# Kernel tuning notes

Hardware: AMD Instinct MI355X
Metric: run time of the kernel (lower is better)

## Reference

```python
import jax, jax.numpy as jnp
import numpy as np

# ---- config (from init_kwargs) ----
PRE_NMS_THRESH = 0.05
PRE_NMS_TOP_N = 1000
NMS_THRESH = 0.6
FPN_POST_NMS_TOP_N = 100
MIN_SIZE = 0.0
FPN_STRIDES = (8.0, 16.0, 32.0, 64.0, 128.0)
TO_REMOVE = 1.0

M = 2097152   # total FPN points over the batch
N = 16        # images
C = 11        # classes incl. background column (zeroed)


def setup_inputs() -> dict:
    key = jax.random.key(0)
    k1, k2, k3, k4, k5, k6 = jax.random.split(key, 6)
    locations = jax.random.uniform(k1, (M, 2), jnp.float32) * 1024.0
    box_cls = jax.random.normal(k2, (M, C), jnp.float32) * 2.0
    box_regression = jax.random.uniform(k3, (M, 4), jnp.float32) * 4.0
    centerness = jax.random.normal(k4, (M, 1), jnp.float32)
    levels = jax.random.randint(k5, (M,), 0, len(FPN_STRIDES), jnp.int32)
    batch_indices = jnp.sort(jax.random.randint(k6, (M,), 0, N, jnp.int32))
    image_sizes = jnp.tile(jnp.array([[800, 1333]], jnp.int32), (N, 1))  # (h, w)
    return dict(locations=locations, levels=levels, batch_indices=batch_indices,
                box_cls=box_cls, box_regression=box_regression,
                centerness=centerness, image_sizes=image_sizes)


def _iou_matrix(b):
    x1, y1, x2, y2 = b[:, 0], b[:, 1], b[:, 2], b[:, 3]
    area = jnp.clip(x2 - x1 + TO_REMOVE, 0.0) * jnp.clip(y2 - y1 + TO_REMOVE, 0.0)
    xx1 = jnp.maximum(x1[:, None], x1[None, :])
    yy1 = jnp.maximum(y1[:, None], y1[None, :])
    xx2 = jnp.minimum(x2[:, None], x2[None, :])
    yy2 = jnp.minimum(y2[:, None], y2[None, :])
    inter = jnp.clip(xx2 - xx1 + TO_REMOVE, 0.0) * jnp.clip(yy2 - yy1 + TO_REMOVE, 0.0)
    return inter / jnp.maximum(area[:, None] + area[None, :] - inter, 1e-9)


def _greedy_nms(iou, keep0):
    # boxes assumed sorted by descending score; keep0 = validity mask
    K = keep0.shape[0]
    idx = jnp.arange(K)
    def step(keep, i):
        sup = (iou[i] > NMS_THRESH) & (idx > i) & keep[i]
        return keep & ~sup, None
    keep, _ = jax.lax.scan(step, keep0, jnp.arange(K))
    return keep


def _fcos_post(locations, box_cls, box_regression, centerness,
               levels, batch_indices, image_sizes):
    strides = jnp.asarray(FPN_STRIDES, box_regression.dtype)
    reg = box_regression * strides[levels][:, None]          # norm_reg_targets=True
    scores = jax.nn.sigmoid(box_cls) * jax.nn.sigmoid(centerness)  # [M,C]
    scores = scores.at[:, -1].set(0.0)                       # kill background column
    boxes_all = jnp.concatenate([locations - reg[:, :2],
                                 locations + reg[:, 2:]], axis=-1)  # [M,4]

    def per_image(args):
        i, hw = args
        m = (batch_indices == i)[:, None] & (scores > PRE_NMS_THRESH)
        flat = jnp.where(m, scores, 0.0).reshape(-1)          # [M*C]
        topv, topi = jax.lax.top_k(flat, PRE_NMS_TOP_N)       # sorted desc
        pt = topi // C
        cl = (topi % C + 1).astype(jnp.int32)                 # labels = class + 1
        b = boxes_all[pt]                                     # [K,4]
        v0 = topv > 0.0                                       # pad entries -> invalid
        sc = jnp.sqrt(jnp.where(v0, topv, 1.0)) * v0          # sqrt(score), safe at pads
        h = hw[0].astype(b.dtype); w = hw[1].astype(b.dtype)
        x1 = jnp.clip(b[:, 0], 0.0, w - TO_REMOVE)            # clip_to_image
        y1 = jnp.clip(b[:, 1], 0.0, h - TO_REMOVE)
        x2 = jnp.clip(b[:, 2], 0.0, w - TO_REMOVE)
        y2 = jnp.clip(b[:, 3], 0.0, h - TO_REMOVE)
        b = jnp.stack([x1, y1, x2, y2], axis=-1)
        ws = x2 - x1 + TO_REMOVE; hs = y2 - y1 + TO_REMOVE    # remove_small_boxes
        keep0 = v0 & (ws >= MIN_SIZE) & (hs >= MIN_SIZE)
        # class-aware NMS via coordinate offset trick
        max_coord = jnp.max(jnp.where(keep0[:, None], b, 0.0))
        boff = jax.lax.stop_gradient(b + (cl.astype(b.dtype) * (max_coord + 1.0))[:, None])
        keep = _greedy_nms(_iou_matrix(boff), keep0)
        sck = jnp.where(keep, sc, 0.0)
        fv, fi = jax.lax.top_k(sck, FPN_POST_NMS_TOP_N)       # fpn_post_nms_top_n
        return b[fi], fv, cl[fi], fv > 0.0

    boxes_o, scores_o, labels_o, valid_o = jax.lax.map(
        per_image, (jnp.arange(N), image_sizes))
    return boxes_o, scores_o, labels_o, valid_o


def reference(locations, levels, batch_indices, box_cls, box_regression,
              centerness, image_sizes):
    return _fcos_post(locations, box_cls, box_regression, centerness,
                      levels, batch_indices, image_sizes)
```

## Files before the change

kernel.cpp:

```cpp
#include <hip/hip_runtime.h>
#include <math.h>

#pragma clang fp contract(off)

#define MPTS   2097152
#define NIMG   16
#define NCLS   11
#define CUTB   0x3F000000u
#define PREB   0x3F4CCC00u
#define BSAFE  620
#define PRECAP 14336
#define NB2    1026
#define NB2P   1040
#define MARG   96u
#define CAP    4096
#define TOPN   1000
#define OUTN   100
#define LCAP   64

typedef unsigned long long u64;

#define SUPW_PER_IMG 8704
__device__ __forceinline__ int chunk_base(int c) {
    return 64 * (16 * c - (c * (c - 1)) / 2);
}

__device__ inline float sigx(float x) {
    float e = (float)exp(-(double)x);
    return 1.0f / (1.0f + e);
}
__device__ inline float sigf(float x) {
    float e = __expf(-x);
    return __builtin_amdgcn_rcpf(1.0f + e);
}
__device__ inline float bfr(float x) {
    unsigned u = __float_as_uint(x);
    unsigned r = (u + 0x7FFFu + ((u >> 16) & 1u)) & 0xFFFF0000u;
    return __uint_as_float(r);
}
__device__ __forceinline__ u64 rdlane64(u64 v, int l) {
    unsigned lo = (unsigned)__builtin_amdgcn_readlane((int)(unsigned)(v & 0xFFFFFFFFull), l);
    unsigned hi = (unsigned)__builtin_amdgcn_readlane((int)(unsigned)(v >> 32), l);
    return ((u64)hi << 32) | (u64)lo;
}

__global__ __launch_bounds__(1024)
void k_hist(const float4* __restrict__ cls4, const float* __restrict__ ctr,
            const int* __restrict__ batch, unsigned* __restrict__ ghist,
            unsigned* __restrict__ gcnt, unsigned* __restrict__ prerec) {
    __shared__ unsigned hist[NB2];
    __shared__ unsigned pA[512], pB[256];
    __shared__ unsigned cA, cB, bA;
    __shared__ int simg;
    const int F4  = MPTS * NCLS / 4;
    const int FPB = F4 / 512;
    int f0 = blockIdx.x * FPB;
    int t = threadIdx.x;
    for (int i = t; i < NB2; i += 1024) hist[i] = 0;
    if (t == 0) { simg = batch[(unsigned)(4u * (unsigned)f0) / NCLS]; cA = 0; cB = 0; }
    __syncthreads();
    int bi = simg;
    unsigned pc = 0xFFFFFFFFu;
    float sfc = 0.0f;
    int bc = 0;
    for (int f = f0 + t; f < f0 + FPB; f += 1024) {
        float4 v = cls4[f];
        float va[4] = {v.x, v.y, v.z, v.w};
        unsigned e0 = 4u * (unsigned)f;
        #pragma unroll
        for (int j = 0; j < 4; j++) {
            float ck = va[j];
            if (ck <= 0.0f) continue;
            unsigned e = e0 + (unsigned)j;
            unsigned p = e / NCLS;
            unsigned k = e - p * NCLS;
            if (k == 10u) continue;
            if (p != pc) {
                pc = p; sfc = sigf(ctr[p]); bc = batch[p];
            }
            unsigned fb = __float_as_uint(sigf(ck) * sfc);
            if (fb < CUTB) continue;
            unsigned bin = (fb - CUTB) >> 13;
            if (bin >= NB2) bin = NB2 - 1;
            if (bc == bi) atomicAdd(&hist[bin], 1u);
            else          atomicAdd(&ghist[(size_t)bc * NB2P + bin], 1u);
            if (fb >= PREB) {
                if (bc == bi) {
                    unsigned sl = atomicAdd(&cA, 1u);
                    if (sl < 512u) pA[sl] = e;
                    else {
                        unsigned pos = atomicAdd(&gcnt[bi * 16 + 8], 1u);
                        if (pos < PRECAP) prerec[(size_t)bi * PRECAP + pos] = e;
                    }
                } else {
                    unsigned sl = atomicAdd(&cB, 1u);
                    if (sl < 256u) pB[sl] = e;
                    else {
                        unsigned pos = atomicAdd(&gcnt[bc * 16 + 8], 1u);
                        if (pos < PRECAP) prerec[(size_t)bc * PRECAP + pos] = e;
                    }
                }
            }
        }
    }
    __syncthreads();
    unsigned* gh = ghist + (size_t)bi * NB2P;
    for (int i = t; i < NB2; i += 1024) {
        unsigned v2 = hist[i];
        if (v2) atomicAdd(&gh[i], v2);
    }
    if (t == 0) {
        unsigned nn = cA; if (nn > 512u) nn = 512u;
        cA = nn;
        bA = nn ? atomicAdd(&gcnt[bi * 16 + 8], nn) : 0u;
    }
    __syncthreads();
    for (unsigned i = t; i < cA; i += 1024) {
        unsigned pos = bA + i;
        if (pos < PRECAP) prerec[(size_t)bi * PRECAP + pos] = pA[i];
    }
    unsigned nb = cB; if (nb > 256u) nb = 256u;
    for (unsigned i = t; i < nb; i += 1024) {
        unsigned e2 = pB[i];
        int img2 = batch[e2 / NCLS];
        unsigned pos = atomicAdd(&gcnt[img2 * 16 + 8], 1u);
        if (pos < PRECAP) prerec[(size_t)img2 * PRECAP + pos] = e2;
    }
}

__global__ void k_thresh(const unsigned* __restrict__ ghist, unsigned* __restrict__ thrbuf,
                         unsigned* __restrict__ gcnt) {
    int img = blockIdx.x;
    const unsigned* h = ghist + (size_t)img * NB2P;
    __shared__ unsigned psum[256];
    int t = threadIdx.x;
    unsigned s = 0;
    int base = t * 5;
    for (int i = 0; i < 5; i++) { int b = base + i; if (b < NB2) s += h[b]; }
    psum[t] = s;
    __syncthreads();
    if (t == 0) {
        unsigned run = 0; int B = 0;
        for (int u = 205; u >= 0; u--) {
            if (run + psum[u] >= (unsigned)TOPN) {
                int btop = u * 5 + 4; if (btop > NB2 - 1) btop = NB2 - 1;
                for (int b = btop; b >= u * 5; b--) {
                    run += h[b];
                    if (run >= (unsigned)TOPN) { B = b; break; }
                }
                break;
            }
            run += psum[u];
        }
        unsigned TB = CUTB + ((unsigned)B << 13) - MARG;
        thrbuf[2 * img] = TB;
        thrbuf[2 * img + 1] = __float_as_uint(__uint_as_float(TB) * 0.998f);
        if (B < BSAFE || gcnt[img * 16 + 8] > PRECAP) atomicOr(&gcnt[1], 1u);
    }
}

__global__ __launch_bounds__(256)
void k_collect(const float4* __restrict__ cls4, const float* __restrict__ clsf,
               const float* __restrict__ ctr, const int* __restrict__ batch,
               const unsigned* __restrict__ thrbuf, unsigned* __restrict__ gcnt,
               const unsigned* __restrict__ prerec, unsigned long long* __restrict__ cand) {
    int t = threadIdx.x;
    if (gcnt[1] == 0u) {
        if (blockIdx.x >= 256) return;
        int img = blockIdx.x >> 4;
        int sub = blockIdx.x & 15;
        unsigned TB = thrbuf[2 * img];
        float scr = __uint_as_float(thrbuf[2 * img + 1]);
        unsigned n = gcnt[img * 16 + 8];
        __shared__ u64 l2[512];
        __shared__ unsigned c2, b2;
        if (t == 0) c2 = 0;
        __syncthreads();
        const unsigned* pr = prerec + (size_t)img * PRECAP;
        for (unsigned i = (unsigned)(sub * 256 + t); i < n; i += 4096) {
            unsigned e = pr[i];
            unsigned p = e / NCLS;
            float ck = clsf[e];
            float cgs = ctr[p];
            float sf = sigf(ck) * sigf(cgs);
            if (sf > scr) {
                float s = sigx(ck) * sigx(cgs);
                unsigned bits = __float_as_uint(s);
                if (bits >= TB && s > 0.05f) {
                    u64 key = ((u64)bits << 32) | (u64)(0xFFFFFFFFu - e);
                    unsigned sl = atomicAdd(&c2, 1u);
                    if (sl < 512u) l2[sl] = key;
                    else {
                        unsigned pos = atomicAdd(&gcnt[img * 16], 1u);
                        if (pos < CAP) cand[(size_t)img * CAP + pos] = key;
                    }
                }
            }
        }
        __syncthreads();
        if (t == 0) {
            unsigned nn = c2; if (nn > 512u) nn = 512u;
            c2 = nn;
            b2 = nn ? atomicAdd(&gcnt[img * 16], nn) : 0u;
        }
        __syncthreads();
        for (unsigned sl = t; sl < c2; sl += 256) {
            unsigned pos = b2 + sl;
            if (pos < CAP) cand[(size_t)img * CAP + pos] = l2[sl];
        }
        return;
    }
    __shared__ unsigned sTB[NIMG];
    __shared__ float sSCR[NIMG];
    __shared__ u64 lbuf[NIMG][LCAP];
    __shared__ unsigned lcnt[NIMG];
    __shared__ unsigned lbase[NIMG];
    if (t < NIMG) {
        sTB[t]  = thrbuf[2 * t];
        sSCR[t] = __uint_as_float(thrbuf[2 * t + 1]);
        lcnt[t] = 0;
    }
    __syncthreads();
    const int F4  = MPTS * NCLS / 4;
    const int FPB = F4 / 2048;
    int f0 = blockIdx.x * FPB;
    unsigned pc = 0xFFFFFFFFu;
    float cgs = 0.0f, sfc = 0.0f, sxc = 0.0f, scrc = 0.0f;
    bool havex = false;
    int bc = 0; unsigned TBc = 0;
    for (int f = f0 + t; f < f0 + FPB; f += 256) {
        float4 v = cls4[f];
        float va[4] = {v.x, v.y, v.z, v.w};
        unsigned e0 = 4u * (unsigned)f;
        #pragma unroll
        for (int j = 0; j < 4; j++) {
            float ck = va[j];
            if (ck <= -0.001f) continue;
            unsigned e = e0 + (unsigned)j;
            unsigned p = e / NCLS;
            unsigned k = e - p * NCLS;
            if (k == 10u) continue;
            if (p != pc) {
                pc = p; cgs = ctr[p]; bc = batch[p];
                sfc = sigf(cgs); havex = false;
                TBc = sTB[bc]; scrc = sSCR[bc];
            }
            float sf = sigf(ck) * sfc;
            if (sf > scrc) {
                if (!havex) { sxc = sigx(cgs); havex = true; }
                float s = sigx(ck) * sxc;
                unsigned bits = __float_as_uint(s);
                if (bits >= TBc && s > 0.05f) {
                    u64 key = ((u64)bits << 32) | (u64)(0xFFFFFFFFu - e);
                    unsigned slot = atomicAdd(&lcnt[bc], 1u);
                    if (slot < LCAP) lbuf[bc][slot] = key;
                    else {
                        unsigned pos = atomicAdd(&gcnt[bc * 16], 1u);
                        if (pos < CAP) cand[(size_t)bc * CAP + pos] = key;
                    }
                }
            }
        }
    }
    __syncthreads();
    if (t < NIMG) {
        unsigned n = lcnt[t]; if (n > LCAP) n = LCAP;
        lcnt[t] = n;
        lbase[t] = n ? atomicAdd(&gcnt[t * 16], n) : 0u;
    }
    __syncthreads();
    for (int s = t; s < NIMG * LCAP; s += 256) {
        int im = s >> 6;
        int sl = s & (LCAP - 1);
        if (sl < (int)lcnt[im]) {
            unsigned pos = lbase[im] + (unsigned)sl;
            if (pos < CAP) cand[(size_t)im * CAP + pos] = lbuf[im][sl];
        }
    }
}

__global__ __launch_bounds__(1024)
void k_rankb(const u64* __restrict__ cand, const unsigned* __restrict__ gcnt,
             const float* __restrict__ loc, const float* __restrict__ breg,
             const int* __restrict__ levels, const int* __restrict__ imsz,
             float* __restrict__ bx, float* __restrict__ sc, int* __restrict__ cl,
             unsigned* __restrict__ k0, float* __restrict__ bo, float* __restrict__ ar) {
    int img = blockIdx.x;
    int t = threadIdx.x;
    __shared__ u64 keys[CAP];
    __shared__ u64 srtl[TOPN];
    __shared__ float red[1024];
    __shared__ float smc;
    unsigned n = gcnt[img * 16]; if (n > CAP) n = CAP;
    for (int i = t; i < (int)n; i += 1024) keys[i] = cand[(size_t)img * CAP + i];
    for (int i = t; i < TOPN; i += 1024) srtl[i] = 0ull;
    __syncthreads();
    for (int ii = t; ii < (int)n; ii += 1024) {
        u64 me = keys[ii];
        int rank = 0;
        int j = 0;
        for (; j + 4 <= (int)n; j += 4) {
            rank += (keys[j]     > me);
            rank += (keys[j + 1] > me);
            rank += (keys[j + 2] > me);
            rank += (keys[j + 3] > me);
        }
        for (; j < (int)n; j++) rank += (keys[j] > me);
        if (rank < TOPN) srtl[rank] = me;
    }
    __syncthreads();
    float wmax = (float)imsz[img * 2 + 1] - 1.0f;
    float hmax = (float)imsz[img * 2 + 0] - 1.0f;
    float lmax = 0.0f;
    for (int r = t; r < TOPN; r += 1024) {
        u64 kv = srtl[r];
        unsigned bits = (unsigned)(kv >> 32);
        unsigned idx = 0xFFFFFFFFu - (unsigned)(kv & 0xFFFFFFFFull);
        float v = __uint_as_float(bits);
        bool v0 = (kv != 0ull) && (v > 0.0f);
        if (!v0) idx = 0;
        unsigned pt = idx / NCLS;
        int c = (int)(idx - pt * NCLS);
        float lx = loc[(size_t)pt * 2 + 0], ly = loc[(size_t)pt * 2 + 1];
        float st = (float)(8 << levels[pt]);
        float r0 = breg[(size_t)pt * 4 + 0] * st;
        float r1 = breg[(size_t)pt * 4 + 1] * st;
        float r2 = breg[(size_t)pt * 4 + 2] * st;
        float r3 = breg[(size_t)pt * 4 + 3] * st;
        float x1 = lx - r0, y1 = ly - r1, x2 = lx + r2, y2 = ly + r3;
        x1 = fminf(fmaxf(x1, 0.0f), wmax);
        y1 = fminf(fmaxf(y1, 0.0f), hmax);
        x2 = fminf(fmaxf(x2, 0.0f), wmax);
        y2 = fminf(fmaxf(y2, 0.0f), hmax);
        float wss = (x2 - x1) + 1.0f, hss = (y2 - y1) + 1.0f;
        bool keep = v0 && (wss >= 0.0f) && (hss >= 0.0f);
        size_t ob = (size_t)img * TOPN + r;
        bx[ob * 4 + 0] = x1; bx[ob * 4 + 1] = y1;
        bx[ob * 4 + 2] = x2; bx[ob * 4 + 3] = y2;
        sc[ob] = v0 ? sqrtf(v) : 0.0f;
        cl[ob] = c + 1;
        k0[ob] = keep ? 1u : 0u;
        if (keep) lmax = fmaxf(lmax, fmaxf(fmaxf(x1, y1), fmaxf(x2, y2)));
    }
    red[t] = lmax; __syncthreads();
    for (int sft = 512; sft > 0; sft >>= 1) {
        if (t < sft) red[t] = fmaxf(red[t], red[t + sft]);
        __syncthreads();
    }
    if (t == 0) smc = red[0];
    __syncthreads();
    float off1 = smc + 1.0f;
    for (int r = t; r < TOPN; r += 1024) {
        size_t ob = (size_t)img * TOPN + r;
        float o = (float)cl[ob] * off1;
        float x1 = bx[ob * 4 + 0] + o, y1 = bx[ob * 4 + 1] + o;
        float x2 = bx[ob * 4 + 2] + o, y2 = bx[ob * 4 + 3] + o;
        bo[ob * 4 + 0] = x1; bo[ob * 4 + 1] = y1;
        bo[ob * 4 + 2] = x2; bo[ob * 4 + 3] = y2;
        float aw = fmaxf((x2 - x1) + 1.0f, 0.0f);
        float ah = fmaxf((y2 - y1) + 1.0f, 0.0f);
        ar[ob] = aw * ah;
    }
}

__global__ __launch_bounds__(1024)
void k_iou(const float* __restrict__ bo, const float* __restrict__ ar,
           u64* __restrict__ sup) {
    int img = blockIdx.x >> 4;
    int c   = blockIdx.x & 15;
    __shared__ float sx1[1024], sy1[1024], sx2[1024], sy2[1024], sa[1024];
    int tid = threadIdx.x;
    {
        int i = tid;
        if (i < TOPN) {
            size_t ob = (size_t)img * TOPN + i;
            sx1[i] = bo[ob * 4 + 0]; sy1[i] = bo[ob * 4 + 1];
            sx2[i] = bo[ob * 4 + 2]; sy2[i] = bo[ob * 4 + 3];
            sa[i]  = ar[ob];
        } else {
            sx1[i] = 0.0f; sy1[i] = 0.0f; sx2[i] = 0.0f; sy2[i] = 0.0f; sa[i] = 0.0f;
        }
    }
    __syncthreads();
    int width = 16 - c;
    int items = 64 * width;
    u64* supc = sup + (size_t)img * SUPW_PER_IMG + chunk_base(c);
    for (int it = tid; it < items; it += 1024) {
        int r  = it & 63;
        int wq = c + (it >> 6);
        int i  = c * 64 + r;
        if (i >= TOPN) continue;
        float x1 = sx1[i], y1 = sy1[i], x2 = sx2[i], y2 = sy2[i], a = sa[i];
        int j0 = wq * 64;
        u64 m = 0ull;
        #pragma unroll 8
        for (int jj = 0; jj < 64; jj++) {
            int j = j0 + jj;
            float xx1 = fmaxf(x1, sx1[j]);
            float yy1 = fmaxf(y1, sy1[j]);
            float xx2 = fminf(x2, sx2[j]);
            float yy2 = fminf(y2, sy2[j]);
            float iw = fmaxf((xx2 - xx1) + 1.0f, 0.0f);
            float ih = fmaxf((yy2 - yy1) + 1.0f, 0.0f);
            float inter = iw * ih;
            float den = fmaxf((a + sa[j]) - inter, 1e-9f);
            if (inter / den > 0.6f) m |= (1ull << jj);
        }
        u64 vm = ~0ull;
        if (wq == c) vm = (r >= 63) ? 0ull : (~0ull << (r + 1));
        int rem = TOPN - j0;
        if (rem < 64) vm &= (rem <= 0) ? 0ull : ((1ull << rem) - 1ull);
        supc[(size_t)r * width + (wq - c)] = m & vm;
    }
}

__device__ __forceinline__ void scan_pref(const u64* __restrict__ supi, int rg, int w, int t,
                                          int C, u64 (&V)[16], u64 &anyV, u64 &dmy) {
    int wd = 16 - C;
    const u64* rb = supi + chunk_base(C) + (rg << 4) * wd - C + w;
    u64 a = 0ull;
    #pragma unroll
    for (int i = 0; i < 16; i++) {
        u64 x = rb[i * wd];
        V[i] = (w >= C) ? x : 0ull;
        a |= V[i];
    }
    anyV = a;
    dmy = supi[chunk_base(C) + (size_t)t * wd];
}

__device__ __forceinline__ void scan_step(int rg, int w, int C,
                                          u64 (&V)[16], u64 anyV, u64 dmy,
                                          u64 &kw_local) {
    u64 m = rdlane64(kw_local, C);
    u64 act = __ballot(dmy != 0ull) & m;
    while (act) {
        int r = __builtin_ctzll(act);
        u64 d = rdlane64(dmy, r);
        m &= ~d;
        act &= act - 1ull;
        act &= m;
    }
    if (__ballot(anyV != 0ull)) {
        u64 loc = 0ull;
        #pragma unroll
        for (int i = 0; i < 16; i++) {
            int row = (rg << 4) + i;
            loc |= V[i] & ((u64)0 - ((m >> row) & 1ull));
        }
        u64 t1 = loc | __shfl_xor(loc, 16);
        u64 t2 = t1 | __shfl_xor(t1, 32);
        kw_local = ((w == C) ? m : kw_local) & ~t2;
    } else if (w == C) {
        kw_local = m;
    }
}

__global__ __launch_bounds__(64)
void k_scan_out(const u64* __restrict__ sup, const unsigned* __restrict__ k0,
                const float* __restrict__ bx, const float* __restrict__ sc,
                const int* __restrict__ cl, float* __restrict__ out) {
    int img = blockIdx.x;
    int t = threadIdx.x;
    int rg = t >> 4, w = t & 15;
    const u64* supi = sup + (size_t)img * SUPW_PER_IMG;

    u64 kw_local = 0ull;
    #pragma unroll
    for (int q = 0; q < 16; q++) {
        int i = (q << 6) + t;
        unsigned vv = (i < TOPN) ? k0[(size_t)img * TOPN + i] : 0u;
        u64 bal = __ballot(vv != 0u);
        if (w == q) kw_local = bal;
    }

    u64 vA[16], vB[16], anyA, anyB, dA, dB;
    scan_pref(supi, rg, w, t, 0, vA, anyA, dA);
    for (int c = 0; c < 16; c += 2) {
        scan_pref(supi, rg, w, t, c + 1, vB, anyB, dB);
        scan_step(rg, w, c, vA, anyA, dA, kw_local);
        if (c + 2 < 16) scan_pref(supi, rg, w, t, c + 2, vA, anyA, dA);
        scan_step(rg, w, c + 1, vB, anyB, dB, kw_local);
    }

    u64 kws[16];
    #pragma unroll
    for (int q = 0; q < 16; q++) kws[q] = rdlane64(kw_local, q);

    __shared__ int fi[OUTN];
    int total_k = 0;
    #pragma unroll
    for (int q = 0; q < 16; q++) total_k += __popcll(kws[q]);
    int snk = total_k < OUTN ? total_k : OUTN;
    int run = 0;
    #pragma unroll
    for (int q = 0; q < 16; q++) {
        u64 word = kws[q];
        int i = (q << 6) + t;
        int kb = __popcll(word & ((1ull << t) - 1ull));
        bool kept = ((word >> t) & 1ull) != 0ull;
        int krank = run + kb;
        if (kept) {
            if (krank < OUTN) fi[krank] = i;
        } else if (i < TOPN) {
            int slot = snk + (i - krank);
            if (slot < OUTN) fi[slot] = i;
        }
        run += __popcll(word);
    }
    __syncthreads();

    for (int q = t; q < OUTN; q += 64) {
        int r = fi[q];
        bool kv = q < snk;
        size_t ob = (size_t)img * TOPN + r;
        float sv = kv ? sc[ob] : 0.0f;
        int o = img * OUTN + q;
        out[o * 4 + 0] = bfr(bx[ob * 4 + 0]);
        out[o * 4 + 1] = bfr(bx[ob * 4 + 1]);
        out[o * 4 + 2] = bfr(bx[ob * 4 + 2]);
        out[o * 4 + 3] = bfr(bx[ob * 4 + 3]);
        out[6400 + o] = bfr(sv);
        out[8000 + o] = (float)cl[ob];
        out[9600 + o] = (sv > 0.0f) ? 1.0f : 0.0f;
    }
}

extern "C" void kernel_launch(void* const* d_in, const int* in_sizes, int n_in,
                              void* d_out, int out_size, void* d_ws, size_t ws_size,
                              hipStream_t stream) {
    const float* loc    = (const float*)d_in[0];
    const int*   levels = (const int*)d_in[1];
    const int*   batch  = (const int*)d_in[2];
    const float* cls    = (const float*)d_in[3];
    const float* breg   = (const float*)d_in[4];
    const float* ctr    = (const float*)d_in[5];
    const int*   imsz   = (const int*)d_in[6];

    char* ws = (char*)d_ws;
    unsigned long long* cand   = (unsigned long long*)(ws + 0);
    unsigned*           ghist  = (unsigned*)(ws + 524288);
    float*              bx     = (float*)(ws + 852096);
    float*              bo     = (float*)(ws + 1108096);
    float*              ar     = (float*)(ws + 1364096);
    float*              sc     = (float*)(ws + 1428096);
    int*                cl     = (int*)(ws + 1492096);
    unsigned*           k0     = (unsigned*)(ws + 1556096);
    unsigned*           gcnt   = (unsigned*)(ws + 1620096);
    unsigned*           thrbuf = (unsigned*)(ws + 1621120);
    u64*                sup    = (u64*)(ws + 1703936);
    unsigned*           prerec = (unsigned*)(ws + 1703936);
    float* out = (float*)d_out;

    hipMemsetAsync(ghist, 0, 16 * NB2P * 4, stream);
    hipMemsetAsync(gcnt, 0, 1024, stream);
    k_hist    <<<512,  1024, 0, stream>>>((const float4*)cls, ctr, batch, ghist, gcnt, prerec);
    k_thresh  <<<16,   256,  0, stream>>>(ghist, thrbuf, gcnt);
    k_collect <<<2048, 256,  0, stream>>>((const float4*)cls, cls, ctr, batch, thrbuf, gcnt, prerec, cand);
    k_rankb   <<<16,   1024, 0, stream>>>(cand, gcnt, loc, breg, levels, imsz,
                                          bx, sc, cl, k0, bo, ar);
    k_iou     <<<256,  1024, 0, stream>>>(bo, ar, sup);
    k_scan_out<<<16,   64,   0, stream>>>(sup, k0, bx, sc, cl, out);
}
```

Baseline: 303.3 us.

## Prune histogram work by centerness bound and fuse threshold into collect

Measured after the change: 316.5 us. 4.3% more time.

```diff
diff --git a/kernel.cpp b/kernel.cpp
--- a/kernel.cpp
+++ b/kernel.cpp
@@ -16,7 +16,6 @@
 #define CAP    4096
 #define TOPN   1000
 #define OUTN   100
-#define LCAP   64
 
 typedef unsigned long long u64;
 
@@ -61,7 +60,8 @@
     __syncthreads();
     int bi = simg;
     unsigned pc = 0xFFFFFFFFu;
-    float sfc = 0.0f;
+    unsigned bcp = 0xFFFFFFFFu;
+    float sfc = 0.0f, Tm = 3.0e38f;
     int bc = 0;
     for (int f = f0 + t; f < f0 + FPB; f += 1024) {
         float4 v = cls4[f];
@@ -69,19 +69,29 @@
         unsigned e0 = 4u * (unsigned)f;
         #pragma unroll
         for (int j = 0; j < 4; j++) {
-            float ck = va[j];
-            if (ck <= 0.0f) continue;
             unsigned e = e0 + (unsigned)j;
             unsigned p = e / NCLS;
             unsigned k = e - p * NCLS;
             if (k == 10u) continue;
             if (p != pc) {
-                pc = p; sfc = sigf(ctr[p]); bc = batch[p];
+                pc = p;
+                float c = ctr[p];
+                if (c > 0.0f) {
+                    float q = sigf(c);
+                    sfc = q;
+                    Tm = (q > 0.50001f) ? (-0.6931472f - __logf(q - 0.5f) - 0.02f)
+                                        : -3.0e38f;
+                } else {
+                    Tm = 3.0e38f; sfc = 0.0f;
+                }
             }
+            float ck = va[j];
+            if (!(ck > Tm)) continue;
             unsigned fb = __float_as_uint(sigf(ck) * sfc);
             if (fb < CUTB) continue;
             unsigned bin = (fb - CUTB) >> 13;
             if (bin >= NB2) bin = NB2 - 1;
+            if (p != bcp) { bcp = p; bc = batch[p]; }
             if (bc == bi) atomicAdd(&hist[bin], 1u);
             else          atomicAdd(&ghist[(size_t)bc * NB2P + bin], 1u);
             if (fb >= PREB) {
@@ -128,54 +138,60 @@
     }
 }
 
-__global__ void k_thresh(const unsigned* __restrict__ ghist, unsigned* __restrict__ thrbuf,
-                         unsigned* __restrict__ gcnt) {
-    int img = blockIdx.x;
-    const unsigned* h = ghist + (size_t)img * NB2P;
+__global__ __launch_bounds__(256)
+void k_collect(const float* __restrict__ clsf, const float* __restrict__ ctr,
+               const int* __restrict__ batch, const unsigned* __restrict__ ghist,
+               unsigned* __restrict__ gcnt, const unsigned* __restrict__ prerec,
+               unsigned long long* __restrict__ cand) {
+    int t = threadIdx.x;
+    int img = blockIdx.x >> 4;
+    int sub = blockIdx.x & 15;
     __shared__ unsigned psum[256];
-    int t = threadIdx.x;
-    unsigned s = 0;
-    int base = t * 5;
-    for (int i = 0; i < 5; i++) { int b = base + i; if (b < NB2) s += h[b]; }
-    psum[t] = s;
-    __syncthreads();
-    if (t == 0) {
-        unsigned run = 0; int B = 0;
-        for (int u = 205; u >= 0; u--) {
-            if (run + psum[u] >= (unsigned)TOPN) {
-                int btop = u * 5 + 4; if (btop > NB2 - 1) btop = NB2 - 1;
-                for (int b = btop; b >= u * 5; b--) {
-                    run += h[b];
-                    if (run >= (unsigned)TOPN) { B = b; break; }
-                }
-                break;
-            }
-            run += psum[u];
-        }
-        unsigned TB = CUTB + ((unsigned)B << 13) - MARG;
-        thrbuf[2 * img] = TB;
-        thrbuf[2 * img + 1] = __float_as_uint(__uint_as_float(TB) * 0.998f);
-        if (B < BSAFE || gcnt[img * 16 + 8] > PRECAP) atomicOr(&gcnt[1], 1u);
-    }
-}
-
-__global__ __launch_bounds__(256)
-void k_collect(const float4* __restrict__ cls4, const float* __restrict__ clsf,
-               const float* __restrict__ ctr, const int* __restrict__ batch,
-               const unsigned* __restrict__ thrbuf, unsigned* __restrict__ gcnt,
-               const unsigned* __restrict__ prerec, unsigned long long* __restrict__ cand) {
-    int t = threadIdx.x;
-    if (gcnt[1] == 0u) {
-        if (blockIdx.x >= 256) return;
-        int img = blockIdx.x >> 4;
-        int sub = blockIdx.x & 15;
-        unsigned TB = thrbuf[2 * img];
-        float scr = __uint_as_float(thrbuf[2 * img + 1]);
-        unsigned n = gcnt[img * 16 + 8];
-        __shared__ u64 l2[512];
-        __shared__ unsigned c2, b2;
+    __shared__ unsigned sTB;
+    __shared__ float sSCR;
+    __shared__ int sSAFE, sPlo, sPhi;
+    __shared__ u64 l2[512];
+    __shared__ unsigned c2, b2;
+    {
+        const unsigned* h = ghist + (size_t)img * NB2P;
+        unsigned s = 0;
+        int base = t * 5;
+        for (int i = 0; i < 5; i++) { int b = base + i; if (b < NB2) s += h[b]; }
+        psum[t] = s;
         if (t == 0) c2 = 0;
         __syncthreads();
+        if (t == 0) {
+            unsigned run = 0; int B = 0;
+            for (int u = 205; u >= 0; u--) {
+                if (run + psum[u] >= (unsigned)TOPN) {
+                    int btop = u * 5 + 4; if (btop > NB2 - 1) btop = NB2 - 1;
+                    for (int b = btop; b >= u * 5; b--) {
+                        run += h[b];
+                        if (run >= (unsigned)TOPN) { B = b; break; }
+                    }
+                    break;
+                }
+                run += psum[u];
+            }
+            unsigned TB = CUTB + ((unsigned)B << 13) - MARG;
+            sTB = TB;
+            sSCR = __uint_as_float(TB) * 0.998f;
+            sSAFE = (B >= BSAFE && gcnt[img * 16 + 8] <= PRECAP) ? 1 : 0;
+            if (!sSAFE) {
+                int lo = 0, hi = MPTS;
+                while (lo < hi) { int m = (lo + hi) >> 1; if (batch[m] < img) lo = m + 1; else hi = m; }
+                sPlo = lo;
+                int lo2 = lo, hi2 = MPTS;
+                while (lo2 < hi2) { int m = (lo2 + hi2) >> 1; if (batch[m] < img + 1) lo2 = m + 1; else hi2 = m; }
+                sPhi = lo2;
+            }
+        }
+        __syncthreads();
+    }
+    unsigned TB = sTB;
+    float scr = sSCR;
+    if (sSAFE) {
+        unsigned n = gcnt[img * 16 + 8];
         const unsigned* pr = prerec + (size_t)img * PRECAP;
         for (unsigned i = (unsigned)(sub * 256 + t); i < n; i += 4096) {
             unsigned e = pr[i];
@@ -208,73 +224,27 @@
             unsigned pos = b2 + sl;
             if (pos < CAP) cand[(size_t)img * CAP + pos] = l2[sl];
         }
-        return;
-    }
-    __shared__ unsigned sTB[NIMG];
-    __shared__ float sSCR[NIMG];
-    __shared__ u64 lbuf[NIMG][LCAP];
-    __shared__ unsigned lcnt[NIMG];
-    __shared__ unsigned lbase[NIMG];
-    if (t < NIMG) {
-        sTB[t]  = thrbuf[2 * t];
-        sSCR[t] = __uint_as_float(thrbuf[2 * t + 1]);
-        lcnt[t] = 0;
-    }
-    __syncthreads();
-    const int F4  = MPTS * NCLS / 4;
-    const int FPB = F4 / 2048;
-    int f0 = blockIdx.x * FPB;
-    unsigned pc = 0xFFFFFFFFu;
-    float cgs = 0.0f, sfc = 0.0f, sxc = 0.0f, scrc = 0.0f;
-    bool havex = false;
-    int bc = 0; unsigned TBc = 0;
-    for (int f = f0 + t; f < f0 + FPB; f += 256) {
-        float4 v = cls4[f];
-        float va[4] = {v.x, v.y, v.z, v.w};
-        unsigned e0 = 4u * (unsigned)f;
-        #pragma unroll
-        for (int j = 0; j < 4; j++) {
-            float ck = va[j];
-            if (ck <= -0.001f) continue;
-            unsigned e = e0 + (unsigned)j;
+    } else {
+        long total_e = (long)(sPhi - sPlo) * NCLS;
+        long ebase = (long)sPlo * NCLS;
+        for (long idx = sub * 256 + t; idx < total_e; idx += 4096) {
+            unsigned e = (unsigned)(ebase + idx);
             unsigned p = e / NCLS;
             unsigned k = e - p * NCLS;
             if (k == 10u) continue;
-            if (p != pc) {
-                pc = p; cgs = ctr[p]; bc = batch[p];
-                sfc = sigf(cgs); havex = false;
-                TBc = sTB[bc]; scrc = sSCR[bc];
-            }
-            float sf = sigf(ck) * sfc;
-            if (sf > scrc) {
-                if (!havex) { sxc = sigx(cgs); havex = true; }
-                float s = sigx(ck) * sxc;
+            float ck = clsf[e];
+            if (ck <= -0.001f) continue;
+            float cgs = ctr[p];
+            float sf = sigf(ck) * sigf(cgs);
+            if (sf > scr) {
+                float s = sigx(ck) * sigx(cgs);
                 unsigned bits = __float_as_uint(s);
-                if (bits >= TBc && s > 0.05f) {
+                if (bits >= TB && s > 0.05f) {
                     u64 key = ((u64)bits << 32) | (u64)(0xFFFFFFFFu - e);
-                    unsigned slot = atomicAdd(&lcnt[bc], 1u);
-                    if (slot < LCAP) lbuf[bc][slot] = key;
-                    else {
-                        unsigned pos = atomicAdd(&gcnt[bc * 16], 1u);
-                        if (pos < CAP) cand[(size_t)bc * CAP + pos] = key;
-                    }
+                    unsigned pos = atomicAdd(&gcnt[img * 16], 1u);
+                    if (pos < CAP) cand[(size_t)img * CAP + pos] = key;
                 }
             }
-        }
-    }
-    __syncthreads();
-    if (t < NIMG) {
-        unsigned n = lcnt[t]; if (n > LCAP) n = LCAP;
-        lcnt[t] = n;
-        lbase[t] = n ? atomicAdd(&gcnt[t * 16], n) : 0u;
-    }
-    __syncthreads();
-    for (int s = t; s < NIMG * LCAP; s += 256) {
-        int im = s >> 6;
-        int sl = s & (LCAP - 1);
-        if (sl < (int)lcnt[im]) {
-            unsigned pos = lbase[im] + (unsigned)sl;
-            if (pos < CAP) cand[(size_t)im * CAP + pos] = lbuf[im][sl];
         }
     }
 }
@@ -540,25 +510,22 @@
     char* ws = (char*)d_ws;
     unsigned long long* cand   = (unsigned long long*)(ws + 0);
     unsigned*           ghist  = (unsigned*)(ws + 524288);
+    unsigned*           gcnt   = (unsigned*)(ws + 590848);
     float*              bx     = (float*)(ws + 852096);
     float*              bo     = (float*)(ws + 1108096);
     float*              ar     = (float*)(ws + 1364096);
     float*              sc     = (float*)(ws + 1428096);
     int*                cl     = (int*)(ws + 1492096);
     unsigned*           k0     = (unsigned*)(ws + 1556096);
-    unsigned*           gcnt   = (unsigned*)(ws + 1620096);
-    unsigned*           thrbuf = (unsigned*)(ws + 1621120);
     u64*                sup    = (u64*)(ws + 1703936);
     unsigned*           prerec = (unsigned*)(ws + 1703936);
     float* out = (float*)d_out;
 
-    hipMemsetAsync(ghist, 0, 16 * NB2P * 4, stream);
-    hipMemsetAsync(gcnt, 0, 1024, stream);
-    k_hist    <<<512,  1024, 0, stream>>>((const float4*)cls, ctr, batch, ghist, gcnt, prerec);
-    k_thresh  <<<16,   256,  0, stream>>>(ghist, thrbuf, gcnt);
-    k_collect <<<2048, 256,  0, stream>>>((const float4*)cls, cls, ctr, batch, thrbuf, gcnt, prerec, cand);
-    k_rankb   <<<16,   1024, 0, stream>>>(cand, gcnt, loc, breg, levels, imsz,
-                                          bx, sc, cl, k0, bo, ar);
-    k_iou     <<<256,  1024, 0, stream>>>(bo, ar, sup);
-    k_scan_out<<<16,   64,   0, stream>>>(sup, k0, bx, sc, cl, out);
-}
+    hipMemsetAsync(ghist, 0, 66560 + 1024, stream);
+    k_hist    <<<512, 1024, 0, stream>>>((const float4*)cls, ctr, batch, ghist, gcnt, prerec);
+    k_collect <<<256, 256,  0, stream>>>(cls, ctr, batch, ghist, gcnt, prerec, cand);
+    k_rankb   <<<16,  1024, 0, stream>>>(cand, gcnt, loc, breg, levels, imsz,
+                                         bx, sc, cl, k0, bo, ar);
+    k_iou     <<<256, 1024, 0, stream>>>(bo, ar, sup);
+    k_scan_out<<<16,  64,   0, stream>>>(sup, k0, bx, sc, cl, out);
+}
```
